# Kernel optimization log

Hardware: AMD Instinct MI355X
Metric: run time of the kernel (lower is better)

## Reference

```python
import jax, jax.numpy as jnp
import numpy as np


def setup_inputs() -> dict:
    key0 = jax.random.key(0)
    k1, k2, k3, k4 = jax.random.split(key0, 4)
    bs, h, S, dk = 4, 16, 2048, 64
    query = jax.random.normal(k1, (bs * h, S, dk), dtype=jnp.float32)
    key = jax.random.normal(k2, (bs * h, S, dk), dtype=jnp.float32)
    value = jax.random.normal(k3, (bs * h, S, dk), dtype=jnp.float32)
    attn_mask = jax.random.randint(k4, (bs, S), 0, 2, dtype=jnp.int64)
    return {"query": query, "key": key, "value": value, "attn_mask": attn_mask}


def reference(query, key, value, attn_mask):
    bs_h, K, dk = key.shape
    Q = query.shape[1]
    bs = attn_mask.shape[0]
    h = bs_h // bs
    # [bs_h, Q, K] scores, scaled by sqrt(d_k)
    scores = jnp.einsum('bqd,bkd->bqk', query, key) / jnp.sqrt(jnp.asarray(dk, query.dtype))
    # mask==0 positions get an additive -1e-10 (faithful to original, incl. its tiny magnitude)
    m = (attn_mask == 0).astype(scores.dtype)          # [bs, K]
    m = jnp.tile(m, (h, 1))[:, None, :]                # [bs_h, 1, K] (torch .repeat(h,1) tiles)
    scores = scores + m * (-1e-10)
    attn = jax.nn.softmax(scores, axis=-1)
    # dropout p=0.0 (identity in this deterministic reference)
    return jnp.einsum('bqk,bkd->bqd', attn, value)
```

## Files before the change

### kernel.cpp

```cpp
#include <hip/hip_runtime.h>
#include <hip/hip_bf16.h>
#include <stdint.h>

typedef __bf16 bf16x8 __attribute__((ext_vector_type(8)));
typedef float  f32x4  __attribute__((ext_vector_type(4)));
typedef float  f32x16 __attribute__((ext_vector_type(16)));
typedef int    i32x2  __attribute__((ext_vector_type(2)));
typedef unsigned short u16x8 __attribute__((ext_vector_type(8)));

#define S_LEN 2048
#define DK    64
#define KVBLK 64
#define NT    (S_LEN / KVBLK)
#define QW    32
#define NWAVE 8
#define QBLK  (QW * NWAVE)
#define TILE_E (KVBLK * DK)

static __device__ __forceinline__ unsigned short f2bf(float f) {
    union { float f; unsigned u; } v; v.f = f;
    unsigned r = v.u + 0x7fffu + ((v.u >> 16) & 1u);
    return (unsigned short)(r >> 16);
}

static __device__ __forceinline__ float fexp2(float x) {
#if __has_builtin(__builtin_amdgcn_exp2f)
    return __builtin_amdgcn_exp2f(x);
#else
    return exp2f(x);
#endif
}

static __device__ __forceinline__ unsigned cvtpk(float lo, float hi) {
    unsigned r;
    asm("v_cvt_pk_bf16_f32 %0, %1, %2" : "=v"(r) : "v"(lo), "v"(hi));
    return r;
}

static __device__ __forceinline__ i32x2 plswap(int a, int b) {
#if __has_builtin(__builtin_amdgcn_permlane32_swap)
    return __builtin_amdgcn_permlane32_swap(a, b, false, false);
#else
    const bool up = (threadIdx.x & 32) != 0;
    int as = __shfl_xor(a, 32, 64);
    int bs = __shfl_xor(b, 32, 64);
    i32x2 r;
    r[0] = up ? bs : a;
    r[1] = up ? b  : as;
    return r;
#endif
}
static __device__ __forceinline__ float xhalf_sum(float x) {
    union { float f; int i; } u; u.f = x;
    i32x2 t = plswap(u.i, u.i);
    union { int i; float f; } a, b; a.i = t[0]; b.i = t[1];
    return a.f + b.f;
}

__global__ __launch_bounds__(256)
void conv_all(const float* __restrict__ Q, const float* __restrict__ K,
              const float* __restrict__ V,
              unsigned short* __restrict__ Qb, unsigned short* __restrict__ Kb,
              unsigned short* __restrict__ Vb, int tiles) {
    __shared__ unsigned short tile[KVBLK][DK + 2];
    const int b = blockIdx.x;
    const int tid = threadIdx.x;
    if (b < tiles) {
        const float* src = K + (size_t)b * TILE_E;
        unsigned short* dst = Kb + (size_t)b * TILE_E;
        #pragma unroll
        for (int g = 0; g < 2; ++g) {
            const int p   = tid * 8 + g * 2048;
            const int f   = p >> 8;
            const int ln  = (p >> 3) & 31;
            const int sub = f >> 3, ds = (f >> 1) & 3, hi = f & 1;
            const float* s = src + (sub * 32 + ln) * DK + ds * 16 + hi * 8;
            u16x8 o;
            #pragma unroll
            for (int j = 0; j < 8; ++j) o[j] = f2bf(s[j]);
            *(u16x8*)&dst[p] = o;
        }
    } else if (b < 2 * tiles) {
        const int bb = b - tiles;
        const float* src = V + (size_t)bb * TILE_E;
        const int k = tid >> 2, c = (tid & 3) * 16;
        #pragma unroll
        for (int j = 0; j < 16; ++j) tile[k][c + j] = f2bf(src[k * DK + c + j]);
        __syncthreads();
        unsigned short* dst = Vb + (size_t)bb * TILE_E;
        #pragma unroll
        for (int g = 0; g < 2; ++g) {
            const int p    = tid * 8 + g * 2048;
            const int g2   = p >> 8;
            const int ln   = (p >> 3) & 31;
            const int hi   = g2 & 1, dblk = (g2 >> 1) & 1, ks = (g2 >> 2) & 1, sub = g2 >> 3;
            const int k0   = sub * 32 + ks * 16 + hi * 8;
            const int d    = dblk * 32 + ln;
            u16x8 o;
            #pragma unroll
            for (int j = 0; j < 8; ++j) o[j] = tile[k0 + j][d];
            *(u16x8*)&dst[p] = o;
        }
    } else {
        const size_t i = ((size_t)(b - 2 * tiles) * 256 + tid) * 8;
        const float4 v0 = *(const float4*)(Q + i);
        const float4 v1 = *(const float4*)(Q + i + 4);
        const float s = 0.125f * 1.44269504089f;
        u16x8 o;
        o[0] = f2bf(v0.x * s); o[1] = f2bf(v0.y * s);
        o[2] = f2bf(v0.z * s); o[3] = f2bf(v0.w * s);
        o[4] = f2bf(v1.x * s); o[5] = f2bf(v1.y * s);
        o[6] = f2bf(v1.z * s); o[7] = f2bf(v1.w * s);
        *(u16x8*)&Qb[i] = o;
    }
}


__global__ __launch_bounds__(512)
void sdpa_fwd2(const unsigned short* __restrict__ Qb,
               const unsigned short* __restrict__ Kb,
               const unsigned short* __restrict__ Vb,
               float* __restrict__ O) {
    __shared__ __align__(16) char smem[49152];

    const int tid  = threadIdx.x;
    const int lane = tid & 63;
    const int wave = tid >> 6;
    const int ln   = lane & 31;
    const int hi   = lane >> 5;

    const int flat = blockIdx.x;
    const int xcd  = flat & 7;
    const int rr   = flat >> 3;
    const int qb_i = rr & 7;
    const int head = (rr >> 3) * 8 + xcd;
    const int q0   = qb_i * QBLK + wave * QW;

    const unsigned short* KbH = Kb + (size_t)head * NT * TILE_E;
    const unsigned short* VbH = Vb + (size_t)head * NT * TILE_E;

    u16x8 qfrag[4];
    {
        const unsigned short* qsrc = Qb + ((size_t)head * S_LEN + q0 + ln) * DK + hi * 8;
        #pragma unroll
        for (int ds = 0; ds < 4; ++ds) qfrag[ds] = *(const u16x8*)&qsrc[ds * 16];
    }

    auto STAGE = [&](int t, int b) {
        const unsigned short* Kt = KbH + (size_t)t * TILE_E;
        const unsigned short* Vt = VbH + (size_t)t * TILE_E;
        unsigned short* sKb = (unsigned short*)(smem + b * 16384);
        unsigned short* sVb = (unsigned short*)(smem + b * 16384 + 8192);
        __builtin_amdgcn_global_load_lds(
            (const __attribute__((address_space(1))) void*)(Kt + tid * 8),
            (__attribute__((address_space(3))) void*)(&sKb[wave * 512]),
            16, 0, 0);
        __builtin_amdgcn_global_load_lds(
            (const __attribute__((address_space(1))) void*)(Vt + tid * 8),
            (__attribute__((address_space(3))) void*)(&sVb[wave * 512]),
            16, 0, 0);
    };

    const int lbase = hi * 512 + ln * 16;

    auto QK = [&](int b, f32x16* s) {
        const char* sK = (const char*)smem + b * 16384 + lbase;
        #pragma unroll
        for (int sub = 0; sub < 2; ++sub)
            #pragma unroll
            for (int r = 0; r < 16; ++r) s[sub][r] = 0.0f;
        __builtin_amdgcn_s_setprio(1);
        #pragma unroll
        for (int sub = 0; sub < 2; ++sub)
            #pragma unroll
            for (int ds = 0; ds < 4; ++ds) {
                u16x8 kf = *(const u16x8*)(sK + sub * 4096 + ds * 1024);
                s[sub] = __builtin_amdgcn_mfma_f32_32x32x16_bf16(
                    __builtin_bit_cast(bf16x8, kf), __builtin_bit_cast(bf16x8, qfrag[ds]),
                    s[sub], 0, 0, 0);
            }
        __builtin_amdgcn_s_setprio(0);
    };

    f32x16 oacc[2];
    #pragma unroll
    for (int dblk = 0; dblk < 2; ++dblk)
        #pragma unroll
        for (int r = 0; r < 16; ++r) oacc[dblk][r] = 0.0f;
    float lsum = 0.0f;

    u16x8 pa[2][2];
    auto SMPACK = [&](f32x16* s) {
        float s0 = 0.f, s1 = 0.f, s2 = 0.f, s3 = 0.f;
        #pragma unroll
        for (int sub = 0; sub < 2; ++sub)
            #pragma unroll
            for (int i = 0; i < 16; i += 4) {
                float e0 = fexp2(s[sub][i]);
                float e1 = fexp2(s[sub][i + 1]);
                float e2 = fexp2(s[sub][i + 2]);
                float e3 = fexp2(s[sub][i + 3]);
                s[sub][i] = e0; s[sub][i + 1] = e1;
                s[sub][i + 2] = e2; s[sub][i + 3] = e3;
                s0 += e0; s1 += e1; s2 += e2; s3 += e3;
            }
        lsum += (s0 + s1) + (s2 + s3);
        #pragma unroll
        for (int sub = 0; sub < 2; ++sub) {
            unsigned w[8];
            #pragma unroll
            for (int i = 0; i < 8; ++i)
                w[i] = cvtpk(s[sub][2 * i], s[sub][2 * i + 1]);
            i32x2 a0 = plswap((int)w[0], (int)w[2]);
            i32x2 a1 = plswap((int)w[1], (int)w[3]);
            i32x2 a2 = plswap((int)w[4], (int)w[6]);
            i32x2 a3 = plswap((int)w[5], (int)w[7]);
            unsigned pk0[4] = { (unsigned)a0[0], (unsigned)a1[0], (unsigned)a0[1], (unsigned)a1[1] };
            unsigned pk1[4] = { (unsigned)a2[0], (unsigned)a3[0], (unsigned)a2[1], (unsigned)a3[1] };
            pa[sub][0] = *(u16x8*)pk0;
            pa[sub][1] = *(u16x8*)pk1;
        }
    };
    auto PV = [&](int b) {
        const char* sVT = (const char*)smem + b * 16384 + 8192 + lbase;
        __builtin_amdgcn_s_setprio(1);
        #pragma unroll
        for (int sub = 0; sub < 2; ++sub)
            #pragma unroll
            for (int dblk = 0; dblk < 2; ++dblk)
                #pragma unroll
                for (int ks = 0; ks < 2; ++ks) {
                    u16x8 vf = *(const u16x8*)(sVT + sub * 4096 + ks * 2048 + dblk * 1024);
                    oacc[dblk] = __builtin_amdgcn_mfma_f32_32x32x16_bf16(
                        __builtin_bit_cast(bf16x8, vf), __builtin_bit_cast(bf16x8, pa[sub][ks]),
                        oacc[dblk], 0, 0, 0);
                }
        __builtin_amdgcn_s_setprio(0);
    };

    STAGE(0, 0);
    asm volatile("s_waitcnt vmcnt(0)" ::: "memory");
    __builtin_amdgcn_s_barrier();
    STAGE(1, 1);
    f32x16 S[2], Snext[2];
    QK(0, S);

    int bPV = 0, bQK = 1, bST = 2;

    for (int t = 0; t < NT - 2; ++t) {
        asm volatile("s_waitcnt vmcnt(0)" ::: "memory");
        __builtin_amdgcn_s_barrier();
        STAGE(t + 2, bST);
        SMPACK(S);
        QK(bQK, Snext);
        PV(bPV);
        S[0] = Snext[0]; S[1] = Snext[1];
        const int tmp = bPV; bPV = bQK; bQK = bST; bST = tmp;
    }

    asm volatile("s_waitcnt vmcnt(0)" ::: "memory");
    __builtin_amdgcn_s_barrier();
    SMPACK(S);
    QK(bQK, Snext);
    PV(bPV);
    S[0] = Snext[0]; S[1] = Snext[1];
    { const int tmp = bPV; bPV = bQK; bQK = bST; bST = tmp; }

    SMPACK(S);
    PV(bPV);

    const float inv = 1.0f / xhalf_sum(lsum);
    #pragma unroll
    for (int ph = 0; ph < 2; ++ph) {
        __syncthreads();
        if ((wave >> 2) == ph) {
            float* tp = (float*)(smem + (wave & 3) * 8192);
            #pragma unroll
            for (int dblk = 0; dblk < 2; ++dblk)
                #pragma unroll
                for (int r = 0; r < 16; ++r) {
                    const int d = dblk * 32 + (r & 3) + 8 * (r >> 2) + 4 * hi;
                    tp[d * 32 + ln] = oacc[dblk][r] * inv;
                }
        }
        __syncthreads();
        if ((wave >> 2) == ph) {
            float* tp = (float*)(smem + (wave & 3) * 8192);
            const int qloc = lane >> 1;
            const int dh   = (lane & 1) * 32;
            float* Orow = O + ((size_t)head * S_LEN + q0 + qloc) * DK + dh;
            #pragma unroll
            for (int c = 0; c < 8; ++c) {
                float4 v;
                v.x = tp[(dh + c * 4 + 0) * 32 + qloc];
                v.y = tp[(dh + c * 4 + 1) * 32 + qloc];
                v.z = tp[(dh + c * 4 + 2) * 32 + qloc];
                v.w = tp[(dh + c * 4 + 3) * 32 + qloc];
                *(float4*)(Orow + c * 4) = v;
            }
        }
    }
}


__global__ __launch_bounds__(256)
void sdpa_fwd_fb(const float* __restrict__ Q, const float* __restrict__ K,
                 const float* __restrict__ V, float* __restrict__ O) {
    __shared__ unsigned short sK[KVBLK * DK];
    __shared__ unsigned short sVT[DK * KVBLK];
    __shared__ unsigned short sP[4][16 * KVBLK];
    const int tid = threadIdx.x, lane = tid & 63, wave = tid >> 6;
    const int lo = lane & 15, hi = lane >> 4;
    const int head = blockIdx.y;
    const int q0 = blockIdx.x * 64 + wave * 16;
    const float* Qh = Q + (size_t)head * S_LEN * DK;
    const float* Kh = K + (size_t)head * S_LEN * DK;
    const float* Vh = V + (size_t)head * S_LEN * DK;
    bf16x8 qfrag[2];
    {
        const int qrow = q0 + lo;
        for (int ks = 0; ks < 2; ++ks) {
            const float* p = Qh + (size_t)qrow * DK + ks * 32 + hi * 8;
            u16x8 u;
            #pragma unroll
            for (int j = 0; j < 8; ++j) u[j] = f2bf(p[j] * 0.125f);
            qfrag[ks] = __builtin_bit_cast(bf16x8, u);
        }
    }
    f32x4 oacc[4];
    #pragma unroll
    for (int dc = 0; dc < 4; ++dc) for (int i = 0; i < 4; ++i) oacc[dc][i] = 0.0f;
    float mrow[4] = {-1e30f, -1e30f, -1e30f, -1e30f};
    float lrow[4] = {0.f, 0.f, 0.f, 0.f};
    for (int kv = 0; kv < S_LEN; kv += KVBLK) {
        {
            const int k = tid >> 2, c = tid & 3;
            const float* src = Kh + (size_t)(kv + k) * DK + c * 16;
            u16x8 a, b;
            #pragma unroll
            for (int j = 0; j < 8; ++j) a[j] = f2bf(src[j]);
            #pragma unroll
            for (int j = 0; j < 8; ++j) b[j] = f2bf(src[8 + j]);
            const int sw = (k & 7) << 3, base = k * DK + c * 16;
            *(u16x8*)&sK[(base) ^ sw] = a;
            *(u16x8*)&sK[(base + 8) ^ sw] = b;
        }
        {
            const int d = tid & 63, sw = (d & 7) << 3;
            #pragma unroll
            for (int half = 0; half < 2; ++half) {
                const int k0 = (tid >> 6) * 8 + half * 32;
                u16x8 v;
                #pragma unroll
                for (int j = 0; j < 8; ++j) v[j] = f2bf(Vh[(size_t)(kv + k0 + j) * DK + d]);
                *(u16x8*)&sVT[(d * KVBLK + k0) ^ sw] = v;
            }
        }
        __syncthreads();
        f32x4 sacc[4];
        #pragma unroll
        for (int kc = 0; kc < 4; ++kc) for (int i = 0; i < 4; ++i) sacc[kc][i] = 0.0f;
        #pragma unroll
        for (int kc = 0; kc < 4; ++kc) {
            const int krow = kc * 16 + lo, sw = (krow & 7) << 3;
            #pragma unroll
            for (int ks = 0; ks < 2; ++ks) {
                u16x8 u = *(const u16x8*)&sK[(krow * DK + ks * 32 + hi * 8) ^ sw];
                sacc[kc] = __builtin_amdgcn_mfma_f32_16x16x32_bf16(
                    qfrag[ks], __builtin_bit_cast(bf16x8, u), sacc[kc], 0, 0, 0);
            }
        }
        float pv[4][4], mnew[4], sc[4];
        #pragma unroll
        for (int r = 0; r < 4; ++r) {
            float t = fmaxf(fmaxf(sacc[0][r], sacc[1][r]), fmaxf(sacc[2][r], sacc[3][r]));
            #pragma unroll
            for (int mm = 1; mm <= 8; mm <<= 1) t = fmaxf(t, __shfl_xor(t, mm, 64));
            mnew[r] = fmaxf(mrow[r], t);
            sc[r] = __expf(mrow[r] - mnew[r]);
        }
        #pragma unroll
        for (int r = 0; r < 4; ++r) {
            float s = 0.f;
            #pragma unroll
            for (int kc = 0; kc < 4; ++kc) { float e = __expf(sacc[kc][r] - mnew[r]); pv[kc][r] = e; s += e; }
            #pragma unroll
            for (int mm = 1; mm <= 8; mm <<= 1) s += __shfl_xor(s, mm, 64);
            lrow[r] = lrow[r] * sc[r] + s;
            mrow[r] = mnew[r];
        }
        #pragma unroll
        for (int dc = 0; dc < 4; ++dc)
            #pragma unroll
            for (int r = 0; r < 4; ++r) oacc[dc][r] *= sc[r];
        unsigned short* sPw = sP[wave];
        #pragma unroll
        for (int r = 0; r < 4; ++r) {
            const int row = hi * 4 + r, sw = (row & 7) << 3;
            #pragma unroll
            for (int kc = 0; kc < 4; ++kc)
                sPw[(row * KVBLK + kc * 16 + lo) ^ sw] = f2bf(pv[kc][r]);
        }
        bf16x8 pfrag[2];
        {
            const int sw = (lo & 7) << 3;
            #pragma unroll
            for (int ks = 0; ks < 2; ++ks) {
                u16x8 u = *(const u16x8*)&sPw[(lo * KVBLK + ks * 32 + hi * 8) ^ sw];
                pfrag[ks] = __builtin_bit_cast(bf16x8, u);
            }
        }
        #pragma unroll
        for (int dc = 0; dc < 4; ++dc) {
            const int d = dc * 16 + lo, sw = (d & 7) << 3;
            #pragma unroll
            for (int ks = 0; ks < 2; ++ks) {
                u16x8 u = *(const u16x8*)&sVT[(d * KVBLK + ks * 32 + hi * 8) ^ sw];
                oacc[dc] = __builtin_amdgcn_mfma_f32_16x16x32_bf16(
                    pfrag[ks], __builtin_bit_cast(bf16x8, u), oacc[dc], 0, 0, 0);
            }
        }
        __syncthreads();
    }
    float* Oh = O + (size_t)head * S_LEN * DK;
    #pragma unroll
    for (int r = 0; r < 4; ++r) {
        const float inv = 1.0f / lrow[r];
        const int row = q0 + hi * 4 + r;
        #pragma unroll
        for (int dc = 0; dc < 4; ++dc)
            Oh[(size_t)row * DK + dc * 16 + lo] = oacc[dc][r] * inv;
    }
}

extern "C" void kernel_launch(void* const* d_in, const int* in_sizes, int n_in,
                              void* d_out, int out_size, void* d_ws, size_t ws_size,
                              hipStream_t stream) {
    const float* Q = (const float*)d_in[0];
    const float* K = (const float*)d_in[1];
    const float* V = (const float*)d_in[2];
    float* O = (float*)d_out;
    const int heads = in_sizes[0] / (S_LEN * DK);
    const size_t n  = (size_t)heads * S_LEN * DK;
    const size_t need = 3 * n * sizeof(unsigned short);

    if (ws_size >= need) {
        unsigned short* Qb = (unsigned short*)d_ws;
        unsigned short* Kb = Qb + n;
        unsigned short* Vb = Kb + n;
        const int tiles = (int)(n / TILE_E);
        const int qblocks = (int)(n / 8 / 256);
        conv_all<<<2 * tiles + qblocks, 256, 0, stream>>>(Q, K, V, Qb, Kb, Vb, tiles);
        sdpa_fwd2<<<heads * (S_LEN / QBLK), 512, 0, stream>>>(Qb, Kb, Vb, O);
    } else {
        dim3 grid(S_LEN / 64, heads);
        sdpa_fwd_fb<<<grid, 256, 0, stream>>>(Q, K, V, O);
    }
}
```

Measured before the change: 102.7 us.

## Split each KV tile across wave pairs and merge partial outputs in LDS

```diff
diff --git a/kernel.cpp b/kernel.cpp
--- a/kernel.cpp
+++ b/kernel.cpp
@@ -14,7 +14,7 @@
 #define NT    (S_LEN / KVBLK)
 #define QW    32
 #define NWAVE 8
-#define QBLK  (QW * NWAVE)
+#define QBLK  128
 #define TILE_E (KVBLK * DK)
 
 static __device__ __forceinline__ unsigned short f2bf(float f) {
@@ -128,13 +128,15 @@
     const int wave = tid >> 6;
     const int ln   = lane & 31;
     const int hi   = lane >> 5;
+    const int qg   = wave >> 1;
+    const int kh   = wave & 1;
 
     const int flat = blockIdx.x;
     const int xcd  = flat & 7;
     const int rr   = flat >> 3;
-    const int qb_i = rr & 7;
-    const int head = (rr >> 3) * 8 + xcd;
-    const int q0   = qb_i * QBLK + wave * QW;
+    const int qb_i = rr & 15;
+    const int head = (rr >> 4) * 8 + xcd;
+    const int q0   = qb_i * QBLK + qg * QW;
 
     const unsigned short* KbH = Kb + (size_t)head * NT * TILE_E;
     const unsigned short* VbH = Vb + (size_t)head * NT * TILE_E;
@@ -163,22 +165,18 @@
 
     const int lbase = hi * 512 + ln * 16;
 
-    auto QK = [&](int b, f32x16* s) {
-        const char* sK = (const char*)smem + b * 16384 + lbase;
-        #pragma unroll
-        for (int sub = 0; sub < 2; ++sub)
-            #pragma unroll
-            for (int r = 0; r < 16; ++r) s[sub][r] = 0.0f;
+    auto QK = [&](int b, f32x16& s) {
+        const char* sK = (const char*)smem + b * 16384 + kh * 4096 + lbase;
+        #pragma unroll
+        for (int r = 0; r < 16; ++r) s[r] = 0.0f;
         __builtin_amdgcn_s_setprio(1);
         #pragma unroll
-        for (int sub = 0; sub < 2; ++sub)
-            #pragma unroll
-            for (int ds = 0; ds < 4; ++ds) {
-                u16x8 kf = *(const u16x8*)(sK + sub * 4096 + ds * 1024);
-                s[sub] = __builtin_amdgcn_mfma_f32_32x32x16_bf16(
-                    __builtin_bit_cast(bf16x8, kf), __builtin_bit_cast(bf16x8, qfrag[ds]),
-                    s[sub], 0, 0, 0);
-            }
+        for (int ds = 0; ds < 4; ++ds) {
+            u16x8 kf = *(const u16x8*)(sK + ds * 1024);
+            s = __builtin_amdgcn_mfma_f32_32x32x16_bf16(
+                __builtin_bit_cast(bf16x8, kf), __builtin_bit_cast(bf16x8, qfrag[ds]),
+                s, 0, 0, 0);
+        }
         __builtin_amdgcn_s_setprio(0);
     };
 
@@ -189,52 +187,43 @@
         for (int r = 0; r < 16; ++r) oacc[dblk][r] = 0.0f;
     float lsum = 0.0f;
 
-    u16x8 pa[2][2];
-    auto SMPACK = [&](f32x16* s) {
+    u16x8 pa[2];
+    auto SMPACK = [&](f32x16& s) {
         float s0 = 0.f, s1 = 0.f, s2 = 0.f, s3 = 0.f;
         #pragma unroll
-        for (int sub = 0; sub < 2; ++sub)
-            #pragma unroll
-            for (int i = 0; i < 16; i += 4) {
-                float e0 = fexp2(s[sub][i]);
-                float e1 = fexp2(s[sub][i + 1]);
-                float e2 = fexp2(s[sub][i + 2]);
-                float e3 = fexp2(s[sub][i + 3]);
-                s[sub][i] = e0; s[sub][i + 1] = e1;
-                s[sub][i + 2] = e2; s[sub][i + 3] = e3;
-                s0 += e0; s1 += e1; s2 += e2; s3 += e3;
-            }
+        for (int i = 0; i < 16; i += 4) {
+            float e0 = fexp2(s[i]);
+            float e1 = fexp2(s[i + 1]);
+            float e2 = fexp2(s[i + 2]);
+            float e3 = fexp2(s[i + 3]);
+            s[i] = e0; s[i + 1] = e1; s[i + 2] = e2; s[i + 3] = e3;
+            s0 += e0; s1 += e1; s2 += e2; s3 += e3;
+        }
         lsum += (s0 + s1) + (s2 + s3);
-        #pragma unroll
-        for (int sub = 0; sub < 2; ++sub) {
-            unsigned w[8];
-            #pragma unroll
-            for (int i = 0; i < 8; ++i)
-                w[i] = cvtpk(s[sub][2 * i], s[sub][2 * i + 1]);
-            i32x2 a0 = plswap((int)w[0], (int)w[2]);
-            i32x2 a1 = plswap((int)w[1], (int)w[3]);
-            i32x2 a2 = plswap((int)w[4], (int)w[6]);
-            i32x2 a3 = plswap((int)w[5], (int)w[7]);
-            unsigned pk0[4] = { (unsigned)a0[0], (unsigned)a1[0], (unsigned)a0[1], (unsigned)a1[1] };
-            unsigned pk1[4] = { (unsigned)a2[0], (unsigned)a3[0], (unsigned)a2[1], (unsigned)a3[1] };
-            pa[sub][0] = *(u16x8*)pk0;
-            pa[sub][1] = *(u16x8*)pk1;
-        }
+        unsigned w[8];
+        #pragma unroll
+        for (int i = 0; i < 8; ++i) w[i] = cvtpk(s[2 * i], s[2 * i + 1]);
+        i32x2 a0 = plswap((int)w[0], (int)w[2]);
+        i32x2 a1 = plswap((int)w[1], (int)w[3]);
+        i32x2 a2 = plswap((int)w[4], (int)w[6]);
+        i32x2 a3 = plswap((int)w[5], (int)w[7]);
+        unsigned pk0[4] = { (unsigned)a0[0], (unsigned)a1[0], (unsigned)a0[1], (unsigned)a1[1] };
+        unsigned pk1[4] = { (unsigned)a2[0], (unsigned)a3[0], (unsigned)a2[1], (unsigned)a3[1] };
+        pa[0] = *(u16x8*)pk0;
+        pa[1] = *(u16x8*)pk1;
     };
     auto PV = [&](int b) {
-        const char* sVT = (const char*)smem + b * 16384 + 8192 + lbase;
+        const char* sVT = (const char*)smem + b * 16384 + 8192 + kh * 4096 + lbase;
         __builtin_amdgcn_s_setprio(1);
         #pragma unroll
-        for (int sub = 0; sub < 2; ++sub)
-            #pragma unroll
-            for (int dblk = 0; dblk < 2; ++dblk)
-                #pragma unroll
-                for (int ks = 0; ks < 2; ++ks) {
-                    u16x8 vf = *(const u16x8*)(sVT + sub * 4096 + ks * 2048 + dblk * 1024);
-                    oacc[dblk] = __builtin_amdgcn_mfma_f32_32x32x16_bf16(
-                        __builtin_bit_cast(bf16x8, vf), __builtin_bit_cast(bf16x8, pa[sub][ks]),
-                        oacc[dblk], 0, 0, 0);
-                }
+        for (int dblk = 0; dblk < 2; ++dblk)
+            #pragma unroll
+            for (int ks = 0; ks < 2; ++ks) {
+                u16x8 vf = *(const u16x8*)(sVT + ks * 2048 + dblk * 1024);
+                oacc[dblk] = __builtin_amdgcn_mfma_f32_32x32x16_bf16(
+                    __builtin_bit_cast(bf16x8, vf), __builtin_bit_cast(bf16x8, pa[ks]),
+                    oacc[dblk], 0, 0, 0);
+            }
         __builtin_amdgcn_s_setprio(0);
     };
 
@@ -242,7 +231,7 @@
     asm volatile("s_waitcnt vmcnt(0)" ::: "memory");
     __builtin_amdgcn_s_barrier();
     STAGE(1, 1);
-    f32x16 S[2], Snext[2];
+    f32x16 S, Snext;
     QK(0, S);
 
     int bPV = 0, bQK = 1, bST = 2;
@@ -254,7 +243,7 @@
         SMPACK(S);
         QK(bQK, Snext);
         PV(bPV);
-        S[0] = Snext[0]; S[1] = Snext[1];
+        S = Snext;
         const int tmp = bPV; bPV = bQK; bQK = bST; bST = tmp;
     }
 
@@ -263,41 +252,50 @@
     SMPACK(S);
     QK(bQK, Snext);
     PV(bPV);
-    S[0] = Snext[0]; S[1] = Snext[1];
+    S = Snext;
     { const int tmp = bPV; bPV = bQK; bQK = bST; bST = tmp; }
 
     SMPACK(S);
     PV(bPV);
 
-    const float inv = 1.0f / xhalf_sum(lsum);
-    #pragma unroll
-    for (int ph = 0; ph < 2; ++ph) {
-        __syncthreads();
-        if ((wave >> 2) == ph) {
-            float* tp = (float*)(smem + (wave & 3) * 8192);
-            #pragma unroll
-            for (int dblk = 0; dblk < 2; ++dblk)
-                #pragma unroll
-                for (int r = 0; r < 16; ++r) {
-                    const int d = dblk * 32 + (r & 3) + 8 * (r >> 2) + 4 * hi;
-                    tp[d * 32 + ln] = oacc[dblk][r] * inv;
-                }
-        }
-        __syncthreads();
-        if ((wave >> 2) == ph) {
-            float* tp = (float*)(smem + (wave & 3) * 8192);
-            const int qloc = lane >> 1;
-            const int dh   = (lane & 1) * 32;
-            float* Orow = O + ((size_t)head * S_LEN + q0 + qloc) * DK + dh;
-            #pragma unroll
-            for (int c = 0; c < 8; ++c) {
-                float4 v;
-                v.x = tp[(dh + c * 4 + 0) * 32 + qloc];
-                v.y = tp[(dh + c * 4 + 1) * 32 + qloc];
-                v.z = tp[(dh + c * 4 + 2) * 32 + qloc];
-                v.w = tp[(dh + c * 4 + 3) * 32 + qloc];
-                *(float4*)(Orow + c * 4) = v;
-            }
+    __syncthreads();
+    const float lh = xhalf_sum(lsum);
+    float* tp = (float*)(smem + qg * 8192);
+    float* ls = (float*)(smem + 32768);
+    if (kh == 1) {
+        #pragma unroll
+        for (int dblk = 0; dblk < 2; ++dblk)
+            #pragma unroll
+            for (int r = 0; r < 16; ++r) {
+                const int d = dblk * 32 + (r & 3) + 8 * (r >> 2) + 4 * hi;
+                tp[d * 32 + ln] = oacc[dblk][r];
+            }
+        if (lane < 32) ls[qg * 32 + ln] = lh;
+    }
+    __syncthreads();
+    if (kh == 0) {
+        const float inv = 1.0f / (lh + ls[qg * 32 + ln]);
+        #pragma unroll
+        for (int dblk = 0; dblk < 2; ++dblk)
+            #pragma unroll
+            for (int r = 0; r < 16; ++r) {
+                const int d = dblk * 32 + (r & 3) + 8 * (r >> 2) + 4 * hi;
+                tp[d * 32 + ln] = (oacc[dblk][r] + tp[d * 32 + ln]) * inv;
+            }
+    }
+    __syncthreads();
+    if (kh == 0) {
+        const int qloc = lane >> 1;
+        const int dh   = (lane & 1) * 32;
+        float* Orow = O + ((size_t)head * S_LEN + q0 + qloc) * DK + dh;
+        #pragma unroll
+        for (int c = 0; c < 8; ++c) {
+            float4 v;
+            v.x = tp[(dh + c * 4 + 0) * 32 + qloc];
+            v.y = tp[(dh + c * 4 + 1) * 32 + qloc];
+            v.z = tp[(dh + c * 4 + 2) * 32 + qloc];
+            v.w = tp[(dh + c * 4 + 3) * 32 + qloc];
+            *(float4*)(Orow + c * 4) = v;
         }
     }
 }
```

Result: slower. 107.0 us (+4.2%).
